# Kernel tuning notes

Hardware: AMD Instinct MI355X
Metric: run time of the kernel (lower is better)

## Reference

```python
import jax, jax.numpy as jnp
import numpy as np

EPS = 1e-12
LAMBDA = 0.5  # kernel['lambda'] for the binary kernel

D, H, Z = 3072, 1024, 32
BS, NN = 128, 32


def setup_inputs() -> dict:
    key = jax.random.key(0)
    ks = jax.random.split(key, 16)
    sc = lambda fan_in: 1.0 / np.sqrt(fan_in)
    inp = {
        "x_c": jax.random.normal(ks[0], (BS, D), jnp.float32),
        "x_nn": jax.random.normal(ks[1], (BS, NN, D), jnp.float32),
        # encoder params: D -> H -> H -> Z
        "We1": jax.random.normal(ks[2], (D, H), jnp.float32) * sc(D),
        "be1": jnp.zeros((H,), jnp.float32),
        "We2": jax.random.normal(ks[3], (H, H), jnp.float32) * sc(H),
        "be2": jnp.zeros((H,), jnp.float32),
        "We3": jax.random.normal(ks[4], (H, Z), jnp.float32) * sc(H),
        "be3": jnp.zeros((Z,), jnp.float32),
        # decoder params: Z -> H -> H -> D
        "Wd1": jax.random.normal(ks[5], (Z, H), jnp.float32) * sc(Z),
        "bd1": jnp.zeros((H,), jnp.float32),
        "Wd2": jax.random.normal(ks[6], (H, H), jnp.float32) * sc(H),
        "bd2": jnp.zeros((H,), jnp.float32),
        "Wd3": jax.random.normal(ks[7], (H, D), jnp.float32) * sc(H),
        "bd3": jnp.zeros((D,), jnp.float32),
    }
    return inp


def _mlp(x, W1, b1, W2, b2, W3, b3):
    h = jax.nn.relu(x @ W1 + b1)
    h = jax.nn.relu(h @ W2 + b2)
    return h @ W3 + b3


def reference(x_c, x_nn, We1, be1, We2, be2, We3, be3,
              Wd1, bd1, Wd2, bd2, Wd3, bd3):
    bs, num_nn, dim = x_nn.shape

    enc = lambda x: _mlp(x, We1, be1, We2, be2, We3, be3)
    dec = lambda z: _mlp(z, Wd1, bd1, Wd2, bd2, Wd3, bd3)

    z_c = enc(x_c)                                   # (bs, Z)
    z_dim = z_c.shape[1]
    z_nn = enc(x_nn.reshape(-1, dim)).reshape(bs, num_nn, z_dim)

    recon = dec(z_c)                                 # (bs, D)
    dz = z_nn - z_c[:, None, :]                      # (bs, nn, Z)
    v = dz.reshape(-1, z_dim)                        # (bs*nn, Z)
    inputs = jnp.broadcast_to(z_c[:, None, :], (bs, num_nn, z_dim)).reshape(-1, z_dim)

    # approx_order == 2: Jacobian-vector and Hessian-bilinear (dz^T H dz) via nested jvp
    jac_fn = lambda z: jax.jvp(dec, (z,), (v,))[1]   # J(z) dz, (bs*nn, D)
    jac, hess = jax.jvp(jac_fn, (inputs,), (v,))     # each (bs*nn, D)

    n_recon = recon[:, None, :] + (jac + 0.5 * hess).reshape(bs, num_nn, dim)

    n_loss = jnp.sum((x_nn - n_recon) ** 2, axis=2)  # ||.||^2, (bs, nn)

    # binary kernel: 1 where neighbor differs from center, lambda where identical
    dist = jnp.linalg.norm(x_c[:, None, :] - x_nn, axis=2)
    weights = jnp.where(dist > EPS, 1.0, LAMBDA)

    loss = jnp.mean(weights * n_loss)
    return loss
```

## Files before the change

### kernel.cpp

```cpp
#include <hip/hip_runtime.h>
#include <math.h>

#define D_DIM 3072
#define H_DIM 1024
#define Z_DIM 32
#define BATCH 128
#define NNEI 32
#define NROWS (BATCH * NNEI)
#define MENC (NROWS + BATCH)

typedef __attribute__((ext_vector_type(8))) short short8;
typedef __attribute__((ext_vector_type(4))) float f32x4;
typedef unsigned short ushortT;

__device__ __forceinline__ unsigned short f2bf(float f) {
  union { float f; unsigned int u; } v; v.f = f;
  unsigned int r = v.u + 0x7FFFu + ((v.u >> 16) & 1u);
  return (unsigned short)(r >> 16);
}
__device__ __forceinline__ float bf2f(unsigned short b) {
  union { unsigned int u; float f; } v; v.u = ((unsigned int)b) << 16;
  return v.f;
}

__device__ __forceinline__ void gl16(const ushortT* g, ushortT* l) {
  typedef __attribute__((address_space(1))) const void gvoid;
  typedef __attribute__((address_space(3))) void lvoid;
  __builtin_amdgcn_global_load_lds((gvoid*)(const void*)g, (lvoid*)(void*)l,
                                   16, 0, 0);
}
#define BAR() asm volatile("s_barrier" ::: "memory")
#define VM0() asm volatile("s_waitcnt vmcnt(0)" ::: "memory")

enum { EP_RELU = 0, EP_BIAS = 1, EP_PART = 2, EP_LOSS = 3 };

template <int MODE, int TN>
__global__ __launch_bounds__(256) __attribute__((amdgpu_waves_per_eu(3)))
void gemm32(
    const ushortT* __restrict__ A, const ushortT* __restrict__ BT,
    const float* __restrict__ bias, ushortT* __restrict__ C,
    float* __restrict__ P, int M, int N, int K, int Ks,
    const ushortT* __restrict__ xa,
    const float* __restrict__ wrow,
    float* __restrict__ out) {
  constexpr int NF = TN / 32;

  __shared__ __align__(16) ushortT As[4096];
  __shared__ __align__(16) ushortT Bs[TN * 32];

  const int t = threadIdx.x;
  const int wave = t >> 6;
  const int lane = t & 63;
  const int quad = lane >> 4;
  const int lm = lane & 15;

  int id = blockIdx.y * gridDim.x + blockIdx.x;
  const int nwg = gridDim.x * gridDim.y;
  if ((nwg & 7) == 0) id = (id & 7) * (nwg >> 3) + (id >> 3);
  const int bm = (id / gridDim.x) * 128;
  const int bn = (id % gridDim.x) * TN;

  const int koff = blockIdx.z * Ks;
  const int wr = (wave >> 1) * 64;
  const int wc = (wave & 1) * (TN / 2);

  f32x4 acc[4][NF];
#pragma unroll
  for (int i = 0; i < 4; ++i)
#pragma unroll
    for (int j = 0; j < NF; ++j) acc[i][j] = (f32x4)0.f;

  const int srow = lane & 15;
  const int skq = lane >> 4;
  const ushortT* gA =
      A + (size_t)(bm + wave * 32 + srow) * K + koff + skq * 8;
  const size_t row16 = (size_t)16 * K;

  const ushortT* gB;
  if (TN == 128) {
    gB = BT + (size_t)(bn + wave * 32 + srow) * K + koff + skq * 8;
  } else if (TN == 64) {
    gB = BT + (size_t)(bn + wave * 16 + srow) * K + koff + skq * 8;
  } else {
    gB = BT + (size_t)(bn + (wave & 1) * 16 + srow) * K + koff + skq * 8;
  }

  ushortT* lA = &As[wave * 1024];
  ushortT* lB = (TN == 128) ? &Bs[wave * 1024] : &Bs[(wave & 1) * 512];

  const int nk = Ks / 32;
  for (int k0 = 0; k0 < nk; ++k0) {
    __syncthreads();
    const size_t o = (size_t)k0 * 32;
    gl16(gA + o, lA);
    gl16(gA + row16 + o, lA + 512);
    if (TN == 128) {
      gl16(gB + o, lB);
      gl16(gB + row16 + o, lB + 512);
    } else if (TN == 64) {
      gl16(gB + o, lB);
    } else {
      if (wave < 2) gl16(gB + o, lB);
    }
    __syncthreads();

    const ushortT* arp = &As[(wr >> 4) * 512 + lane * 8];
    const ushortT* brp = &Bs[(wc >> 4) * 512 + lane * 8];
    short8 af[4], bf[NF];
#pragma unroll
    for (int mt = 0; mt < 4; ++mt) af[mt] = *(const short8*)(arp + mt * 512);
#pragma unroll
    for (int nt = 0; nt < NF; ++nt) bf[nt] = *(const short8*)(brp + nt * 512);
#pragma unroll
    for (int mt = 0; mt < 4; ++mt)
#pragma unroll
      for (int nt = 0; nt < NF; ++nt)
        acc[mt][nt] = __builtin_amdgcn_mfma_f32_16x16x32_bf16(
            af[mt], bf[nt], acc[mt][nt], 0, 0, 0);
  }

  if (MODE == EP_LOSS) {
    __shared__ float red[256];
    float lsum = 0.f;
#pragma unroll
    for (int mt = 0; mt < 4; ++mt) {
#pragma unroll
      for (int r = 0; r < 4; ++r) {
        const int row = bm + wr + mt * 16 + quad * 4 + r;
        const float w = wrow[row];
        const ushortT* xr = xa + (size_t)row * N;
        float rs = 0.f;
#pragma unroll
        for (int nt = 0; nt < NF; ++nt) {
          const int col = bn + wc + nt * 16 + lm;
          const float d = bf2f(xr[col]) - (acc[mt][nt][r] + bias[col]);
          rs = fmaf(d, d, rs);
        }
        lsum = fmaf(w, rs, lsum);
      }
    }
    __syncthreads();
    red[t] = lsum;
    __syncthreads();
    for (int st = 128; st > 0; st >>= 1) {
      if (t < st) red[t] += red[t + st];
      __syncthreads();
    }
    if (t == 0) atomicAdd(out, red[0] * (1.0f / (float)NROWS));
  } else if (MODE == EP_PART) {
#pragma unroll
    for (int mt = 0; mt < 4; ++mt)
#pragma unroll
      for (int r = 0; r < 4; ++r) {
        const int row = bm + wr + mt * 16 + quad * 4 + r;
#pragma unroll
        for (int nt = 0; nt < NF; ++nt) {
          const int col = bn + wc + nt * 16 + lm;
          P[((size_t)blockIdx.z * M + row) * N + col] = acc[mt][nt][r];
        }
      }
  } else {
#pragma unroll
    for (int mt = 0; mt < 4; ++mt)
#pragma unroll
      for (int r = 0; r < 4; ++r) {
        const int row = bm + wr + mt * 16 + quad * 4 + r;
#pragma unroll
        for (int nt = 0; nt < NF; ++nt) {
          const int col = bn + wc + nt * 16 + lm;
          float v = acc[mt][nt][r] + bias[col];
          if (MODE == EP_RELU) v = fmaxf(v, 0.f);
          C[(size_t)row * N + col] = f2bf(v);
        }
      }
  }
}

template <int MODE, int TN>
__global__ __launch_bounds__(256) void gemm_sb(
    const ushortT* __restrict__ A, const ushortT* __restrict__ BT,
    const float* __restrict__ bias, ushortT* __restrict__ C,
    int M, int N, int K,
    const ushortT* __restrict__ xa, const float* __restrict__ wrow,
    float* __restrict__ out) {
  constexpr int NF = TN / 32;
  __shared__ __align__(16) ushortT As[4096];
  __shared__ __align__(16) ushortT Bs[TN * 32];

  const int t = threadIdx.x;
  const int wave = t >> 6;
  const int lane = t & 63;
  const int quad = lane >> 4;
  const int lm = lane & 15;

  int id = blockIdx.y * gridDim.x + blockIdx.x;
  const int nwg = gridDim.x * gridDim.y;
  if ((nwg & 7) == 0) id = (id & 7) * (nwg >> 3) + (id >> 3);
  const int bm = (id / gridDim.x) * 128;
  const int bn = (id % gridDim.x) * TN;

  const int wr = (wave >> 1) * 64;
  const int wc = (wave & 1) * (TN / 2);

  const int a_r0 = (t >> 6) * 16 + (t & 15);
  const int a_q8 = ((t >> 4) & 3) * 8;
  const ushortT* ga0 = A + (size_t)(bm + a_r0) * K + a_q8;
  const ushortT* gb0 = BT + (size_t)(bn + a_r0) * K + a_q8;

  ushortT* asw = &As[wave * 512];
  ushortT* bsw = &Bs[wave * 512];
  gl16(ga0, asw);
  gl16(ga0 + (size_t)64 * K, asw + 2048);
  gl16(gb0, bsw);
  if (TN == 128) gl16(gb0 + (size_t)64 * K, bsw + 2048);
  VM0();
  BAR();

  f32x4 acc[4][NF];
#pragma unroll
  for (int i = 0; i < 4; ++i)
#pragma unroll
    for (int j = 0; j < NF; ++j) acc[i][j] = (f32x4)0.f;

  const ushortT* arp = As + (wr >> 4) * 512 + lane * 8;
  const ushortT* brp = Bs + (wc >> 4) * 512 + lane * 8;
  short8 af[4], bf[NF];
#pragma unroll
  for (int mt = 0; mt < 4; ++mt) af[mt] = *(const short8*)(arp + mt * 512);
#pragma unroll
  for (int nt = 0; nt < NF; ++nt) bf[nt] = *(const short8*)(brp + nt * 512);
#pragma unroll
  for (int mt = 0; mt < 4; ++mt)
#pragma unroll
    for (int nt = 0; nt < NF; ++nt)
      acc[mt][nt] = __builtin_amdgcn_mfma_f32_16x16x32_bf16(
          af[mt], bf[nt], acc[mt][nt], 0, 0, 0);

#pragma unroll
  for (int mt = 0; mt < 4; ++mt)
#pragma unroll
    for (int r = 0; r < 4; ++r) {
      const int row = bm + wr + mt * 16 + quad * 4 + r;
#pragma unroll
      for (int nt = 0; nt < NF; ++nt) {
        const int col = bn + wc + nt * 16 + lm;
        float v = acc[mt][nt][r] + bias[col];
        if (MODE == EP_RELU) v = fmaxf(v, 0.f);
        C[(size_t)row * N + col] = f2bf(v);
      }
    }
}

template <int S, int RELU>
__global__ __launch_bounds__(256) void reduce_lin(
    const float* __restrict__ P, const float* __restrict__ bias,
    ushortT* __restrict__ outp, int MN, int Nmask) {
  const int i4 = (blockIdx.x * 256 + threadIdx.x) * 4;
  if (i4 >= MN) return;
  float4 s = *(const float4*)(P + i4);
#pragma unroll
  for (int k = 1; k < S; ++k) {
    const float4 q = *(const float4*)(P + (size_t)k * MN + i4);
    s.x += q.x; s.y += q.y; s.z += q.z; s.w += q.w;
  }
  const float4 b = *(const float4*)(bias + (i4 & Nmask));
  float vx = s.x + b.x, vy = s.y + b.y, vz = s.z + b.z, vw = s.w + b.w;
  if (RELU) {
    vx = fmaxf(vx, 0.f); vy = fmaxf(vy, 0.f);
    vz = fmaxf(vz, 0.f); vw = fmaxf(vw, 0.f);
  }
  ushort4 o;
  o.x = f2bf(vx); o.y = f2bf(vy); o.z = f2bf(vz); o.w = f2bf(vw);
  *(ushort4*)(outp + i4) = o;
}

__global__ __launch_bounds__(256) void mask_apply(
    const ushortT* __restrict__ U, ushortT* __restrict__ outp) {
  const int i4 = (blockIdx.x * 256 + threadIdx.x) * 4;
  const int r = i4 >> 10;
  const int c = i4 & 1023;
  ushort4 u = *(const ushort4*)(U + i4);
  ushort4 o;
  if (r < NROWS) {
    const ushort4 m = *(const ushort4*)(U + (((size_t)(NROWS + (r >> 5))) << 10) + c);
    o.x = ((short)m.x > 0) ? u.x : 0;
    o.y = ((short)m.y > 0) ? u.y : 0;
    o.z = ((short)m.z > 0) ? u.z : 0;
    o.w = ((short)m.w > 0) ? u.w : 0;
  } else {
    o.x = ((short)u.x > 0) ? u.x : 0;
    o.y = ((short)u.y > 0) ? u.y : 0;
    o.z = ((short)u.z > 0) ? u.z : 0;
    o.w = ((short)u.w > 0) ? u.w : 0;
  }
  *(ushort4*)(outp + i4) = o;
}

__global__ __launch_bounds__(256) void prep_kernel(
    const float* __restrict__ x_c, const float* __restrict__ x_nn,
    ushortT* __restrict__ A_enc, float* __restrict__ wbuf, float* __restrict__ out) {
  const int i = blockIdx.x;
  const int t = threadIdx.x;
  if (i < NROWS) {
    const float* src = x_nn + (size_t)i * D_DIM;
    const float* ctr = x_c + (size_t)(i >> 5) * D_DIM;
    ushortT* dst = A_enc + (size_t)i * D_DIM;
    float s = 0.f;
    for (int d = t * 4; d < D_DIM; d += 1024) {
      const float4 v = *(const float4*)(src + d);
      const float4 c = *(const float4*)(ctr + d);
      ushort4 o;
      o.x = f2bf(v.x); o.y = f2bf(v.y); o.z = f2bf(v.z); o.w = f2bf(v.w);
      *(ushort4*)(dst + d) = o;
      const float dx = v.x - c.x, dy = v.y - c.y, dz = v.z - c.z, dw = v.w - c.w;
      s += dx * dx + dy * dy + dz * dz + dw * dw;
    }
    __shared__ float red[256];
    red[t] = s;
    __syncthreads();
    for (int st = 128; st > 0; st >>= 1) {
      if (t < st) red[t] += red[t + st];
      __syncthreads();
    }
    if (t == 0) {
      wbuf[i] = (red[0] > 1e-24f) ? 1.0f : 0.5f;
      if (i == 0) out[0] = 0.f;
    }
  } else {
    const int r = i - NROWS;
    const float* src = x_c + (size_t)r * D_DIM;
    ushortT* dst = A_enc + (size_t)i * D_DIM;
    for (int d = t * 4; d < D_DIM; d += 1024) {
      const float4 v = *(const float4*)(src + d);
      ushort4 o;
      o.x = f2bf(v.x); o.y = f2bf(v.y); o.z = f2bf(v.z); o.w = f2bf(v.w);
      *(ushort4*)(dst + d) = o;
    }
  }
}

__global__ __launch_bounds__(256) void trans_all(
    const float* __restrict__ We1, const float* __restrict__ We2,
    const float* __restrict__ We3, const float* __restrict__ Wd1,
    const float* __restrict__ Wd2, const float* __restrict__ Wd3,
    ushortT* __restrict__ We1T, ushortT* __restrict__ We2T,
    ushortT* __restrict__ We3T, ushortT* __restrict__ Wd1T,
    ushortT* __restrict__ Wd2T, ushortT* __restrict__ Wd3T) {
  const int b = blockIdx.x;
  const float* W; ushortT* WT; int K, N, loc;
  if (b < 3072)      { W = We1; WT = We1T; K = 3072; N = 1024; loc = b; }
  else if (b < 4096) { W = We2; WT = We2T; K = 1024; N = 1024; loc = b - 3072; }
  else if (b < 4128) { W = We3; WT = We3T; K = 1024; N = 32;   loc = b - 4096; }
  else if (b < 4160) { W = Wd1; WT = Wd1T; K = 32;   N = 1024; loc = b - 4128; }
  else if (b < 5184) { W = Wd2; WT = Wd2T; K = 1024; N = 1024; loc = b - 4160; }
  else               { W = Wd3; WT = Wd3T; K = 1024; N = 3072; loc = b - 5184; }
  const int ntiles = N >> 5;
  const int n0 = (loc % ntiles) * 32;
  const int k0 = (loc / ntiles) * 32;
  __shared__ float tile[32][33];
  const int tx = threadIdx.x & 31;
  const int ty = threadIdx.x >> 5;
  for (int i = ty; i < 32; i += 8)
    tile[i][tx] = W[(size_t)(k0 + i) * N + n0 + tx];
  __syncthreads();
  for (int i = ty; i < 32; i += 8)
    WT[(size_t)(n0 + i) * K + k0 + tx] = f2bf(tile[tx][i]);
}

extern "C" void kernel_launch(void* const* d_in, const int* in_sizes, int n_in,
                              void* d_out, int out_size, void* d_ws, size_t ws_size,
                              hipStream_t stream) {
  const float* x_c = (const float*)d_in[0];
  const float* x_nn = (const float*)d_in[1];
  const float* We1 = (const float*)d_in[2];
  const float* be1 = (const float*)d_in[3];
  const float* We2 = (const float*)d_in[4];
  const float* be2 = (const float*)d_in[5];
  const float* We3 = (const float*)d_in[6];
  const float* be3 = (const float*)d_in[7];
  const float* Wd1 = (const float*)d_in[8];
  const float* bd1 = (const float*)d_in[9];
  const float* Wd2 = (const float*)d_in[10];
  const float* bd2 = (const float*)d_in[11];
  const float* Wd3 = (const float*)d_in[12];
  const float* bd3 = (const float*)d_in[13];
  float* out = (float*)d_out;

  char* p = (char*)d_ws;
  auto alloc = [&](size_t bytes) {
    char* r = p;
    p += (bytes + 255) & ~(size_t)255;
    return r;
  };
  ushortT* We1T = (ushortT*)alloc((size_t)H_DIM * D_DIM * 2);
  ushortT* We2T = (ushortT*)alloc((size_t)H_DIM * H_DIM * 2);
  ushortT* We3T = (ushortT*)alloc((size_t)Z_DIM * H_DIM * 2);
  ushortT* Wd1T = (ushortT*)alloc((size_t)H_DIM * Z_DIM * 2);
  ushortT* Wd2T = (ushortT*)alloc((size_t)H_DIM * H_DIM * 2);
  ushortT* Wd3T = (ushortT*)alloc((size_t)D_DIM * H_DIM * 2);
  ushortT* A_enc = (ushortT*)alloc((size_t)MENC * D_DIM * 2);
  ushortT* bufX = (ushortT*)alloc((size_t)MENC * H_DIM * 2);
  ushortT* bufY = (ushortT*)alloc((size_t)MENC * H_DIM * 2);
  ushortT* z = (ushortT*)alloc((size_t)MENC * Z_DIM * 2);
  float* Pbig = (float*)alloc((size_t)3 * MENC * H_DIM * 4);
  float* wbuf = (float*)alloc((size_t)NROWS * 4);

  const dim3 blk(256);
  const float* nofp = nullptr;
  const ushortT* nobf = nullptr;

  prep_kernel<<<dim3(MENC), blk, 0, stream>>>(x_c, x_nn, A_enc, wbuf, out);
  trans_all<<<dim3(8256), blk, 0, stream>>>(We1, We2, We3, Wd1, Wd2, Wd3,
                                            We1T, We2T, We3T, Wd1T, Wd2T, Wd3T);

  gemm32<EP_PART, 128><<<dim3(8, 33, 3), blk, 0, stream>>>(
      A_enc, We1T, nofp, nullptr, Pbig, MENC, H_DIM, D_DIM, D_DIM / 3,
      nobf, nofp, nullptr);
  reduce_lin<3, 1><<<dim3((MENC * H_DIM) / 1024), blk, 0, stream>>>(
      Pbig, be1, bufX, MENC * H_DIM, H_DIM - 1);

  gemm32<EP_PART, 128><<<dim3(8, 33, 2), blk, 0, stream>>>(
      bufX, We2T, nofp, nullptr, Pbig, MENC, H_DIM, H_DIM, H_DIM / 2,
      nobf, nofp, nullptr);
  reduce_lin<2, 1><<<dim3((MENC * H_DIM) / 1024), blk, 0, stream>>>(
      Pbig, be2, bufY, MENC * H_DIM, H_DIM - 1);

  gemm32<EP_PART, 32><<<dim3(1, 33, 8), blk, 0, stream>>>(
      bufY, We3T, nofp, nullptr, Pbig, MENC, Z_DIM, H_DIM, H_DIM / 8,
      nobf, nofp, nullptr);
  reduce_lin<8, 0><<<dim3((MENC * Z_DIM) / 1024), blk, 0, stream>>>(
      Pbig, be3, z, MENC * Z_DIM, Z_DIM - 1);

  gemm_sb<EP_BIAS, 64><<<dim3(16, 33), blk, 0, stream>>>(
      z, Wd1T, bd1, bufX, MENC, H_DIM, Z_DIM, nobf, nofp, nullptr);
  mask_apply<<<dim3((MENC * H_DIM) / 1024), blk, 0, stream>>>(bufX, bufY);
  gemm32<EP_PART, 128><<<dim3(8, 33, 2), blk, 0, stream>>>(
      bufY, Wd2T, nofp, nullptr, Pbig, MENC, H_DIM, H_DIM, H_DIM / 2,
      nobf, nofp, nullptr);
  reduce_lin<2, 0><<<dim3((MENC * H_DIM) / 1024), blk, 0, stream>>>(
      Pbig, bd2, bufX, MENC * H_DIM, H_DIM - 1);
  mask_apply<<<dim3((NROWS * H_DIM) / 1024), blk, 0, stream>>>(bufX, bufY);
  gemm32<EP_LOSS, 128><<<dim3(24, 32, 1), blk, 0, stream>>>(
      bufY, Wd3T, bd3, nullptr, nullptr, NROWS, D_DIM, H_DIM, H_DIM,
      A_enc, wbuf, out);
}
```

Baseline: 381.1 us.

## Add 4-stage LDS ring buffer with async prefetch three tiles ahead in GEMM

```diff
diff --git a/kernel.cpp b/kernel.cpp
--- a/kernel.cpp
+++ b/kernel.cpp
@@ -32,10 +32,20 @@
 #define BAR() asm volatile("s_barrier" ::: "memory")
 #define VM0() asm volatile("s_waitcnt vmcnt(0)" ::: "memory")
 
+template <int N>
+__device__ __forceinline__ void vmw() {
+  if constexpr (N == 0)      asm volatile("s_waitcnt vmcnt(0)" ::: "memory");
+  else if constexpr (N == 2) asm volatile("s_waitcnt vmcnt(2)" ::: "memory");
+  else if constexpr (N == 3) asm volatile("s_waitcnt vmcnt(3)" ::: "memory");
+  else if constexpr (N == 4) asm volatile("s_waitcnt vmcnt(4)" ::: "memory");
+  else if constexpr (N == 6) asm volatile("s_waitcnt vmcnt(6)" ::: "memory");
+  else if constexpr (N == 8) asm volatile("s_waitcnt vmcnt(8)" ::: "memory");
+}
+
 enum { EP_RELU = 0, EP_BIAS = 1, EP_PART = 2, EP_LOSS = 3 };
 
 template <int MODE, int TN>
-__global__ __launch_bounds__(256) __attribute__((amdgpu_waves_per_eu(3)))
+__global__ __launch_bounds__(256) __attribute__((amdgpu_waves_per_eu(2)))
 void gemm32(
     const ushortT* __restrict__ A, const ushortT* __restrict__ BT,
     const float* __restrict__ bias, ushortT* __restrict__ C,
@@ -45,8 +55,8 @@
     float* __restrict__ out) {
   constexpr int NF = TN / 32;
 
-  __shared__ __align__(16) ushortT As[4096];
-  __shared__ __align__(16) ushortT Bs[TN * 32];
+  __shared__ __align__(16) ushortT As[4][4096];
+  __shared__ __align__(16) ushortT Bs[4][TN * 32];
 
   const int t = threadIdx.x;
   const int wave = t >> 6;
@@ -85,27 +95,46 @@
     gB = BT + (size_t)(bn + (wave & 1) * 16 + srow) * K + koff + skq * 8;
   }
 
-  ushortT* lA = &As[wave * 1024];
-  ushortT* lB = (TN == 128) ? &Bs[wave * 1024] : &Bs[(wave & 1) * 512];
+#define STAGE(kk, sl)                                           \
+  {                                                             \
+    const size_t o = (size_t)(kk) * 32;                         \
+    ushortT* lA = &As[sl][wave * 1024];                         \
+    gl16(gA + o, lA);                                           \
+    gl16(gA + row16 + o, lA + 512);                             \
+    if (TN == 128) {                                            \
+      ushortT* lB = &Bs[sl][wave * 1024];                       \
+      gl16(gB + o, lB);                                         \
+      gl16(gB + row16 + o, lB + 512);                           \
+    } else if (TN == 64) {                                      \
+      gl16(gB + o, &Bs[sl][wave * 512]);                        \
+    } else {                                                    \
+      if (wave < 2) gl16(gB + o, &Bs[sl][(wave & 1) * 512]);    \
+    }                                                           \
+  }
 
   const int nk = Ks / 32;
-  for (int k0 = 0; k0 < nk; ++k0) {
-    __syncthreads();
-    const size_t o = (size_t)k0 * 32;
-    gl16(gA + o, lA);
-    gl16(gA + row16 + o, lA + 512);
+  for (int p = 0; p < 3 && p < nk; ++p) STAGE(p, p);
+
+  for (int t0 = 0; t0 < nk; ++t0) {
+    const int sl = t0 & 3;
+    const int ahead = nk - 1 - t0;
+    const int a2 = ahead >= 2 ? 2 : ahead;
     if (TN == 128) {
-      gl16(gB + o, lB);
-      gl16(gB + row16 + o, lB + 512);
+      if (a2 == 2) vmw<8>(); else if (a2 == 1) vmw<4>(); else vmw<0>();
     } else if (TN == 64) {
-      gl16(gB + o, lB);
+      if (a2 == 2) vmw<6>(); else if (a2 == 1) vmw<3>(); else vmw<0>();
     } else {
-      if (wave < 2) gl16(gB + o, lB);
-    }
-    __syncthreads();
-
-    const ushortT* arp = &As[(wr >> 4) * 512 + lane * 8];
-    const ushortT* brp = &Bs[(wc >> 4) * 512 + lane * 8];
+      if (wave < 2) {
+        if (a2 == 2) vmw<6>(); else if (a2 == 1) vmw<3>(); else vmw<0>();
+      } else {
+        if (a2 == 2) vmw<4>(); else if (a2 == 1) vmw<2>(); else vmw<0>();
+      }
+    }
+    BAR();
+    if (t0 + 3 < nk) STAGE(t0 + 3, (t0 + 3) & 3);
+
+    const ushortT* arp = &As[sl][(wr >> 4) * 512 + lane * 8];
+    const ushortT* brp = &Bs[sl][(wc >> 4) * 512 + lane * 8];
     short8 af[4], bf[NF];
 #pragma unroll
     for (int mt = 0; mt < 4; ++mt) af[mt] = *(const short8*)(arp + mt * 512);
@@ -118,6 +147,7 @@
         acc[mt][nt] = __builtin_amdgcn_mfma_f32_16x16x32_bf16(
             af[mt], bf[nt], acc[mt][nt], 0, 0, 0);
   }
+#undef STAGE
 
   if (MODE == EP_LOSS) {
     __shared__ float red[256];
```

New measurement: 405.7 us. 1.06x slower.
